# Optimization experiments

Measured on AMD Instinct MI355X. Metric: run time of the kernel, lower is better.

## Reference

```python
import jax, jax.numpy as jnp
import numpy as np


def setup_inputs() -> dict:
    key = jax.random.key(0)
    ks = jax.random.split(key, 7)
    B, P, D = 4, 2048, 1024
    s = 1.0 / np.sqrt(D)
    return {
        "x":  jax.random.normal(ks[0], (B, P, D), dtype=jnp.float32),
        "Wq": jax.random.normal(ks[1], (D, D), dtype=jnp.float32) * s,
        "bq": jnp.zeros((D,), dtype=jnp.float32),
        "Wk": jax.random.normal(ks[2], (D, D), dtype=jnp.float32) * s,
        "bk": jnp.zeros((D,), dtype=jnp.float32),
        "Wv": jax.random.normal(ks[3], (D, D), dtype=jnp.float32) * s,
        "bv": jnp.zeros((D,), dtype=jnp.float32),
    }


def reference(x, Wq, bq, Wk, bk, Wv, bv):
    # x: [B, P, D]; Linear uses W stored torch-style [out, in]: y = x @ W.T + b
    b, p, d = x.shape
    q = jnp.einsum("bpd,ed->bpe", x, Wq) + bq
    k = jnp.einsum("bpd,ed->bpe", x, Wk) + bk
    v = jnp.einsum("bpd,ed->bpe", x, Wv) + bv
    attn = jnp.einsum("bqd,bkd->bqk", q, k)  # [B, P, P]
    causal = jnp.triu(jnp.ones((p, p), dtype=bool), k=1)  # True above diagonal
    attn = jnp.where(causal, -jnp.inf, attn)
    attn = attn / jnp.sqrt(jnp.asarray(d, dtype=attn.dtype))
    scores = jax.nn.softmax(attn, axis=-1)
    # dropout is identity in eval/deterministic mode
    return jnp.einsum("bqk,bkd->bqd", scores, v)
```

## Files before the change

### kernel.cpp

```cpp
#include <hip/hip_runtime.h>
#include <hip/hip_bf16.h>


typedef __attribute__((ext_vector_type(8))) short bf16x8;
typedef __attribute__((ext_vector_type(4))) float f32x4;

__device__ __forceinline__ unsigned short f2bf(float f) {
    union { float f; unsigned u; } v; v.f = f;
    unsigned r = v.u + 0x7FFF + ((v.u >> 16) & 1);
    return (unsigned short)(r >> 16);
}

__device__ __forceinline__ void gload_lds16(const unsigned short* g, unsigned short* l) {
    __builtin_amdgcn_global_load_lds(
        (const __attribute__((address_space(1))) unsigned int*)g,
        (__attribute__((address_space(3))) unsigned int*)l, 16, 0, 0);
}

__global__ void convert_kernel(const float* __restrict__ x,  const float* __restrict__ wq,
                               const float* __restrict__ wk, const float* __restrict__ wv,
                               const float* __restrict__ bq, const float* __restrict__ bk,
                               const float* __restrict__ bv,
                               unsigned short* __restrict__ xb, unsigned short* __restrict__ wqkvb,
                               float* __restrict__ bqkv, float* __restrict__ lsum) {
    long t = (long)blockIdx.x * blockDim.x + threadIdx.x;
    long idx = t * 4;
    const float* src; unsigned short* dst; long off;
    if      (idx <  8388608) { src = x;  dst = xb;            off = idx;            }
    else if (idx <  9437184) { src = wq; dst = wqkvb;         off = idx -  8388608; }
    else if (idx < 10485760) { src = wk; dst = wqkvb+1048576; off = idx -  9437184; }
    else if (idx < 11534336) { src = wv; dst = wqkvb+2097152; off = idx - 10485760; }
    else return;
    float4 v = *(const float4*)(src + off);
    ushort4 o = make_ushort4(f2bf(v.x), f2bf(v.y), f2bf(v.z), f2bf(v.w));
    *(ushort4*)(dst + off) = o;
    if (t < 768) {
        long o2 = t * 4;
        float4 b;
        if      (o2 < 1024) b = *(const float4*)(bq + o2);
        else if (o2 < 2048) b = *(const float4*)(bk + o2 - 1024);
        else                b = *(const float4*)(bv + o2 - 2048);
        *(float4*)(bqkv + o2) = b;
    }
    if (t >= 1024 && t < 3072) {
        float4 z = make_float4(0.f, 0.f, 0.f, 0.f);
        *(float4*)(lsum + (t - 1024) * 4) = z;
    }
}

template<int MODE>
__global__ __launch_bounds__(256)
void gemm_bt(const unsigned short* __restrict__ A, int lda,
             const unsigned short* __restrict__ B, int ldb,
             unsigned short* __restrict__ Cb, float* __restrict__ Cf, int ldc,
             unsigned short* __restrict__ VTb,
             const float* __restrict__ bias_col, float* __restrict__ lsum,
             int K, long bsA, long bsB, long bsC, long bsL) {
    int m0, n0, z;
    if (MODE == 1) {
        const int t = blockIdx.x;
        int i = (int)((sqrtf(8.0f * t + 1.0f) - 1.0f) * 0.5f);
        while ((i + 1) * (i + 2) / 2 <= t) ++i;
        while (i * (i + 1) / 2 > t) --i;
        const int j = t - i * (i + 1) / 2;
        m0 = i * 128; n0 = j * 128; z = blockIdx.y;
    } else {
        n0 = blockIdx.x * 128; m0 = blockIdx.y * 128; z = blockIdx.z;
    }
    A += (long)z * bsA;
    B += (long)z * bsB;
    if (MODE == 2) Cf += (long)z * bsC; else Cb += (long)z * bsC;
    if (MODE != 0) lsum += (long)z * bsL;

    const int Keff = (MODE == 2) ? (m0 + 128) : K;

    __shared__ unsigned short As[128 * 64];
    __shared__ unsigned short Bs[128 * 64];

    const int tid  = threadIdx.x;
    const int lane = tid & 63;
    const int w    = tid >> 6;
    const int wr   = (w >> 1) * 64;
    const int wc   = (w & 1) * 64;
    const int q    = lane >> 4;
    const int ln   = lane & 15;

    const int srow = lane >> 3;
    const int sc   = (lane & 7) ^ srow;
    const unsigned short* gA = A + (long)(m0 + w * 32 + srow) * lda + sc * 8;
    const unsigned short* gB = B + (long)(n0 + w * 32 + srow) * ldb + sc * 8;

    const int pr0 = ((q)     ^ (ln & 7)) * 8;
    const int pr1 = ((q + 4) ^ (ln & 7)) * 8;

    f32x4 acc[4][4] = {};

    for (int k0 = 0; k0 < Keff; k0 += 64) {
        __syncthreads();
#pragma unroll
        for (int s = 0; s < 4; ++s) {
            gload_lds16(gA + k0 + (long)(s * 8) * lda, &As[(w * 32 + s * 8) * 64]);
            gload_lds16(gB + k0 + (long)(s * 8) * ldb, &Bs[(w * 32 + s * 8) * 64]);
        }
        __syncthreads();
#pragma unroll
        for (int kk = 0; kk < 2; ++kk) {
            const int pr = kk ? pr1 : pr0;
            bf16x8 af[4], bfr[4];
#pragma unroll
            for (int i = 0; i < 4; ++i)
                af[i] = *(const bf16x8*)(&As[(wr + i * 16 + ln) * 64 + pr]);
#pragma unroll
            for (int j = 0; j < 4; ++j)
                bfr[j] = *(const bf16x8*)(&Bs[(wc + j * 16 + ln) * 64 + pr]);
#pragma unroll
            for (int i = 0; i < 4; ++i)
#pragma unroll
                for (int j = 0; j < 4; ++j)
                    acc[i][j] = __builtin_amdgcn_mfma_f32_16x16x32_bf16(bfr[j], af[i], acc[i][j], 0, 0, 0);
        }
    }

    if (MODE == 0) {
        if (n0 < 2048) {
#pragma unroll
            for (int j = 0; j < 4; ++j) {
                const float4 bc = *(const float4*)(bias_col + n0 + wc + j * 16 + q * 4);
#pragma unroll
                for (int i = 0; i < 4; ++i) {
                    const int m = m0 + wr + i * 16 + ln;
                    const int n = n0 + wc + j * 16 + q * 4;
                    ushort4 o = make_ushort4(f2bf(acc[i][j][0] + bc.x), f2bf(acc[i][j][1] + bc.y),
                                             f2bf(acc[i][j][2] + bc.z), f2bf(acc[i][j][3] + bc.w));
                    *(ushort4*)(Cb + (long)m * ldc + n) = o;
                }
            }
        } else {
#pragma unroll
            for (int j = 0; j < 4; ++j) {
                const float4 bc = *(const float4*)(bias_col + n0 + wc + j * 16 + q * 4);
                const int e = n0 - 2048 + wc + j * 16 + q * 4;
#pragma unroll
                for (int i = 0; i < 4; ++i) {
                    const int m = m0 + wr + i * 16 + ln;
                    VTb[(long)(e    ) * 8192 + m] = f2bf(acc[i][j][0] + bc.x);
                    VTb[(long)(e + 1) * 8192 + m] = f2bf(acc[i][j][1] + bc.y);
                    VTb[(long)(e + 2) * 8192 + m] = f2bf(acc[i][j][2] + bc.z);
                    VTb[(long)(e + 3) * 8192 + m] = f2bf(acc[i][j][3] + bc.w);
                }
            }
        }
    } else if (MODE == 1) {
        const float scale = 0.03125f;
        float rs[4] = {0.f, 0.f, 0.f, 0.f};
#pragma unroll
        for (int i = 0; i < 4; ++i) {
            const int m = m0 + wr + i * 16 + ln;
#pragma unroll
            for (int j = 0; j < 4; ++j) {
                const int n = n0 + wc + j * 16 + q * 4;
                float p0 = (n     <= m) ? __expf(acc[i][j][0] * scale) : 0.f;
                float p1 = (n + 1 <= m) ? __expf(acc[i][j][1] * scale) : 0.f;
                float p2 = (n + 2 <= m) ? __expf(acc[i][j][2] * scale) : 0.f;
                float p3 = (n + 3 <= m) ? __expf(acc[i][j][3] * scale) : 0.f;
                rs[i] += (p0 + p1) + (p2 + p3);
                ushort4 o = make_ushort4(f2bf(p0), f2bf(p1), f2bf(p2), f2bf(p3));
                *(ushort4*)(Cb + (long)m * ldc + n) = o;
            }
        }
#pragma unroll
        for (int i = 0; i < 4; ++i) {
            float s = rs[i];
            s += __shfl_xor(s, 16); s += __shfl_xor(s, 32);
            if (lane < 16) atomicAdd(&lsum[m0 + wr + i * 16 + ln], s);
        }
    } else {
#pragma unroll
        for (int i = 0; i < 4; ++i) {
            const int m = m0 + wr + i * 16 + ln;
            const float inv = 1.0f / lsum[m];
#pragma unroll
            for (int j = 0; j < 4; ++j) {
                const int n = n0 + wc + j * 16 + q * 4;
                float4 o = make_float4(acc[i][j][0] * inv, acc[i][j][1] * inv,
                                       acc[i][j][2] * inv, acc[i][j][3] * inv);
                *(float4*)(Cf + (long)m * ldc + n) = o;
            }
        }
    }
}

extern "C" void kernel_launch(void* const* d_in, const int* in_sizes, int n_in,
                              void* d_out, int out_size, void* d_ws, size_t ws_size,
                              hipStream_t stream) {
    const float* x  = (const float*)d_in[0];
    const float* Wq = (const float*)d_in[1];
    const float* bq = (const float*)d_in[2];
    const float* Wk = (const float*)d_in[3];
    const float* bk = (const float*)d_in[4];
    const float* Wv = (const float*)d_in[5];
    const float* bv = (const float*)d_in[6];
    float* out = (float*)d_out;

    char* ws = (char*)d_ws;
    unsigned short* xb    = (unsigned short*)ws; ws += (long)8192 * 1024 * 2;
    unsigned short* wqkvb = (unsigned short*)ws; ws += (long)3072 * 1024 * 2;
    float*          bqkv  = (float*)ws;          ws += (long)3072 * 4;
    float*          lsum  = (float*)ws;          ws += (long)8192 * 4;
    unsigned short* QKb   = (unsigned short*)ws; ws += (long)8192 * 2048 * 2;
    unsigned short* VTb   = (unsigned short*)ws; ws += (long)1024 * 8192 * 2;
    unsigned short* Pb    = (unsigned short*)ws; ws += (long)4 * 2048 * 2048 * 2;

    hipLaunchKernelGGL(convert_kernel, dim3(11264), dim3(256), 0, stream,
                       x, Wq, Wk, Wv, bq, bk, bv, xb, wqkvb, bqkv, lsum);

    hipLaunchKernelGGL((gemm_bt<0>), dim3(24, 64, 1), dim3(256), 0, stream,
                       xb, 1024, wqkvb, 1024, QKb, (float*)nullptr, 2048, VTb,
                       bqkv, (float*)nullptr, 1024, 0L, 0L, 0L, 0L);

    hipLaunchKernelGGL((gemm_bt<1>), dim3(136, 4, 1), dim3(256), 0, stream,
                       QKb, 2048, QKb + 1024, 2048, Pb, (float*)nullptr, 2048,
                       (unsigned short*)nullptr, (const float*)nullptr, lsum,
                       1024, (long)2048 * 2048, (long)2048 * 2048, (long)2048 * 2048, 2048L);

    hipLaunchKernelGGL((gemm_bt<2>), dim3(8, 16, 4), dim3(256), 0, stream,
                       Pb, 2048, VTb, 8192, (unsigned short*)nullptr, out, 1024,
                       (unsigned short*)nullptr, (const float*)nullptr, lsum,
                       2048, (long)2048 * 2048, 2048L, (long)2048 * 1024, 2048L);
}
```

Measured before the change: 264.6 us.

## Enlarge GEMM tiles to 256x128 and transpose V via swapped MFMA operands

All three GEMM phases now use 256x128 block tiles, with each wave owning 64 rows across the full 128 columns, so every loaded B fragment is reused across more accumulators. The triangular tile enumeration for the QK^T phase is redone for 256-row strips, and the grids are halved to match. The V projection swaps the MFMA operand order so the transposed result can be written as contiguous ushort4 stores instead of scattered scalar stores. The costs are double the accumulator registers (launch bounds now request 2 blocks), fewer blocks per grid, and coarser causal tiles that compute more masked work on the diagonal.

```diff
diff --git a/kernel.cpp b/kernel.cpp
--- a/kernel.cpp
+++ b/kernel.cpp
@@ -48,8 +48,47 @@
     }
 }
 
+template<bool SWAP>
+__device__ __forceinline__ void kloop(const unsigned short* gA, int lda,
+                                      const unsigned short* gB, int ldb,
+                                      unsigned short* As, unsigned short* Bs,
+                                      int w, int lane, int Keff, f32x4 (&acc)[4][8]) {
+    const int q  = lane >> 4;
+    const int ln = lane & 15;
+    const int pr0 = ((q)     ^ (ln & 7)) * 8;
+    const int pr1 = ((q + 4) ^ (ln & 7)) * 8;
+    for (int k0 = 0; k0 < Keff; k0 += 64) {
+        __syncthreads();
+#pragma unroll
+        for (int s = 0; s < 8; ++s)
+            gload_lds16(gA + k0 + (long)(s * 8) * lda, &As[(w * 64 + s * 8) * 64]);
+#pragma unroll
+        for (int s = 0; s < 4; ++s)
+            gload_lds16(gB + k0 + (long)(s * 8) * ldb, &Bs[(w * 32 + s * 8) * 64]);
+        __syncthreads();
+#pragma unroll
+        for (int kk = 0; kk < 2; ++kk) {
+            const int pr = kk ? pr1 : pr0;
+            bf16x8 af[4], bfr[8];
+#pragma unroll
+            for (int i = 0; i < 4; ++i)
+                af[i] = *(const bf16x8*)(&As[(w * 64 + i * 16 + ln) * 64 + pr]);
+#pragma unroll
+            for (int j = 0; j < 8; ++j)
+                bfr[j] = *(const bf16x8*)(&Bs[(j * 16 + ln) * 64 + pr]);
+#pragma unroll
+            for (int i = 0; i < 4; ++i)
+#pragma unroll
+                for (int j = 0; j < 8; ++j)
+                    acc[i][j] = SWAP
+                        ? __builtin_amdgcn_mfma_f32_16x16x32_bf16(bfr[j], af[i], acc[i][j], 0, 0, 0)
+                        : __builtin_amdgcn_mfma_f32_16x16x32_bf16(af[i], bfr[j], acc[i][j], 0, 0, 0);
+        }
+    }
+}
+
 template<int MODE>
-__global__ __launch_bounds__(256)
+__global__ __launch_bounds__(256, 2)
 void gemm_bt(const unsigned short* __restrict__ A, int lda,
              const unsigned short* __restrict__ B, int ldb,
              unsigned short* __restrict__ Cb, float* __restrict__ Cf, int ldc,
@@ -59,129 +98,97 @@
     int m0, n0, z;
     if (MODE == 1) {
         const int t = blockIdx.x;
-        int i = (int)((sqrtf(8.0f * t + 1.0f) - 1.0f) * 0.5f);
-        while ((i + 1) * (i + 2) / 2 <= t) ++i;
-        while (i * (i + 1) / 2 > t) --i;
-        const int j = t - i * (i + 1) / 2;
-        m0 = i * 128; n0 = j * 128; z = blockIdx.y;
+        int i = (int)sqrtf((float)t);
+        while (i * i + i > t) --i;
+        while ((i + 1) * (i + 1) + (i + 1) <= t) ++i;
+        const int j = t - i * i - i;
+        m0 = i * 256; n0 = j * 128; z = blockIdx.y;
     } else {
-        n0 = blockIdx.x * 128; m0 = blockIdx.y * 128; z = blockIdx.z;
+        n0 = blockIdx.x * 128; m0 = blockIdx.y * 256; z = blockIdx.z;
     }
     A += (long)z * bsA;
     B += (long)z * bsB;
     if (MODE == 2) Cf += (long)z * bsC; else Cb += (long)z * bsC;
     if (MODE != 0) lsum += (long)z * bsL;
 
-    const int Keff = (MODE == 2) ? (m0 + 128) : K;
-
-    __shared__ unsigned short As[128 * 64];
-    __shared__ unsigned short Bs[128 * 64];
+    const int Keff = (MODE == 2) ? (m0 + 256) : K;
+
+    __shared__ __align__(16) unsigned short As[256 * 64];
+    __shared__ __align__(16) unsigned short Bs[128 * 64];
 
     const int tid  = threadIdx.x;
     const int lane = tid & 63;
     const int w    = tid >> 6;
-    const int wr   = (w >> 1) * 64;
-    const int wc   = (w & 1) * 64;
     const int q    = lane >> 4;
     const int ln   = lane & 15;
 
     const int srow = lane >> 3;
     const int sc   = (lane & 7) ^ srow;
-    const unsigned short* gA = A + (long)(m0 + w * 32 + srow) * lda + sc * 8;
+    const unsigned short* gA = A + (long)(m0 + w * 64 + srow) * lda + sc * 8;
     const unsigned short* gB = B + (long)(n0 + w * 32 + srow) * ldb + sc * 8;
 
-    const int pr0 = ((q)     ^ (ln & 7)) * 8;
-    const int pr1 = ((q + 4) ^ (ln & 7)) * 8;
-
-    f32x4 acc[4][4] = {};
-
-    for (int k0 = 0; k0 < Keff; k0 += 64) {
-        __syncthreads();
-#pragma unroll
-        for (int s = 0; s < 4; ++s) {
-            gload_lds16(gA + k0 + (long)(s * 8) * lda, &As[(w * 32 + s * 8) * 64]);
-            gload_lds16(gB + k0 + (long)(s * 8) * ldb, &Bs[(w * 32 + s * 8) * 64]);
-        }
-        __syncthreads();
-#pragma unroll
-        for (int kk = 0; kk < 2; ++kk) {
-            const int pr = kk ? pr1 : pr0;
-            bf16x8 af[4], bfr[4];
-#pragma unroll
-            for (int i = 0; i < 4; ++i)
-                af[i] = *(const bf16x8*)(&As[(wr + i * 16 + ln) * 64 + pr]);
-#pragma unroll
-            for (int j = 0; j < 4; ++j)
-                bfr[j] = *(const bf16x8*)(&Bs[(wc + j * 16 + ln) * 64 + pr]);
-#pragma unroll
-            for (int i = 0; i < 4; ++i)
-#pragma unroll
-                for (int j = 0; j < 4; ++j)
-                    acc[i][j] = __builtin_amdgcn_mfma_f32_16x16x32_bf16(bfr[j], af[i], acc[i][j], 0, 0, 0);
-        }
-    }
+    f32x4 acc[4][8] = {};
+
+    if (MODE == 0 && n0 >= 2048) {
+        kloop<false>(gA, lda, gB, ldb, As, Bs, w, lane, Keff, acc);
+#pragma unroll
+        for (int j = 0; j < 8; ++j) {
+            const int e = n0 - 2048 + j * 16 + ln;
+            const float bc = bias_col[n0 + j * 16 + ln];
+#pragma unroll
+            for (int i = 0; i < 4; ++i) {
+                const int m = m0 + w * 64 + i * 16 + q * 4;
+                ushort4 o = make_ushort4(f2bf(acc[i][j][0] + bc), f2bf(acc[i][j][1] + bc),
+                                         f2bf(acc[i][j][2] + bc), f2bf(acc[i][j][3] + bc));
+                *(ushort4*)(VTb + (long)e * 8192 + m) = o;
+            }
+        }
+        return;
+    }
+
+    kloop<true>(gA, lda, gB, ldb, As, Bs, w, lane, Keff, acc);
 
     if (MODE == 0) {
-        if (n0 < 2048) {
-#pragma unroll
-            for (int j = 0; j < 4; ++j) {
-                const float4 bc = *(const float4*)(bias_col + n0 + wc + j * 16 + q * 4);
-#pragma unroll
-                for (int i = 0; i < 4; ++i) {
-                    const int m = m0 + wr + i * 16 + ln;
-                    const int n = n0 + wc + j * 16 + q * 4;
-                    ushort4 o = make_ushort4(f2bf(acc[i][j][0] + bc.x), f2bf(acc[i][j][1] + bc.y),
-                                             f2bf(acc[i][j][2] + bc.z), f2bf(acc[i][j][3] + bc.w));
-                    *(ushort4*)(Cb + (long)m * ldc + n) = o;
-                }
-            }
-        } else {
-#pragma unroll
-            for (int j = 0; j < 4; ++j) {
-                const float4 bc = *(const float4*)(bias_col + n0 + wc + j * 16 + q * 4);
-                const int e = n0 - 2048 + wc + j * 16 + q * 4;
-#pragma unroll
-                for (int i = 0; i < 4; ++i) {
-                    const int m = m0 + wr + i * 16 + ln;
-                    VTb[(long)(e    ) * 8192 + m] = f2bf(acc[i][j][0] + bc.x);
-                    VTb[(long)(e + 1) * 8192 + m] = f2bf(acc[i][j][1] + bc.y);
-                    VTb[(long)(e + 2) * 8192 + m] = f2bf(acc[i][j][2] + bc.z);
-                    VTb[(long)(e + 3) * 8192 + m] = f2bf(acc[i][j][3] + bc.w);
-                }
+#pragma unroll
+        for (int j = 0; j < 8; ++j) {
+            const float4 bc = *(const float4*)(bias_col + n0 + j * 16 + q * 4);
+#pragma unroll
+            for (int i = 0; i < 4; ++i) {
+                const int m = m0 + w * 64 + i * 16 + ln;
+                const int n = n0 + j * 16 + q * 4;
+                ushort4 o = make_ushort4(f2bf(acc[i][j][0] + bc.x), f2bf(acc[i][j][1] + bc.y),
+                                         f2bf(acc[i][j][2] + bc.z), f2bf(acc[i][j][3] + bc.w));
+                *(ushort4*)(Cb + (long)m * ldc + n) = o;
             }
         }
     } else if (MODE == 1) {
         const float scale = 0.03125f;
-        float rs[4] = {0.f, 0.f, 0.f, 0.f};
 #pragma unroll
         for (int i = 0; i < 4; ++i) {
-            const int m = m0 + wr + i * 16 + ln;
-#pragma unroll
-            for (int j = 0; j < 4; ++j) {
-                const int n = n0 + wc + j * 16 + q * 4;
+            const int m = m0 + w * 64 + i * 16 + ln;
+            float rs = 0.f;
+#pragma unroll
+            for (int j = 0; j < 8; ++j) {
+                const int n = n0 + j * 16 + q * 4;
                 float p0 = (n     <= m) ? __expf(acc[i][j][0] * scale) : 0.f;
                 float p1 = (n + 1 <= m) ? __expf(acc[i][j][1] * scale) : 0.f;
                 float p2 = (n + 2 <= m) ? __expf(acc[i][j][2] * scale) : 0.f;
                 float p3 = (n + 3 <= m) ? __expf(acc[i][j][3] * scale) : 0.f;
-                rs[i] += (p0 + p1) + (p2 + p3);
+                rs += (p0 + p1) + (p2 + p3);
                 ushort4 o = make_ushort4(f2bf(p0), f2bf(p1), f2bf(p2), f2bf(p3));
                 *(ushort4*)(Cb + (long)m * ldc + n) = o;
             }
-        }
+            rs += __shfl_xor(rs, 16); rs += __shfl_xor(rs, 32);
+            if (lane < 16) atomicAdd(&lsum[m], rs);
+        }
+    } else {
 #pragma unroll
         for (int i = 0; i < 4; ++i) {
-            float s = rs[i];
-            s += __shfl_xor(s, 16); s += __shfl_xor(s, 32);
-            if (lane < 16) atomicAdd(&lsum[m0 + wr + i * 16 + ln], s);
-        }
-    } else {
-#pragma unroll
-        for (int i = 0; i < 4; ++i) {
-            const int m = m0 + wr + i * 16 + ln;
+            const int m = m0 + w * 64 + i * 16 + ln;
             const float inv = 1.0f / lsum[m];
 #pragma unroll
-            for (int j = 0; j < 4; ++j) {
-                const int n = n0 + wc + j * 16 + q * 4;
+            for (int j = 0; j < 8; ++j) {
+                const int n = n0 + j * 16 + q * 4;
                 float4 o = make_float4(acc[i][j][0] * inv, acc[i][j][1] * inv,
                                        acc[i][j][2] * inv, acc[i][j][3] * inv);
                 *(float4*)(Cf + (long)m * ldc + n) = o;
@@ -214,16 +221,16 @@
     hipLaunchKernelGGL(convert_kernel, dim3(11264), dim3(256), 0, stream,
                        x, Wq, Wk, Wv, bq, bk, bv, xb, wqkvb, bqkv, lsum);
 
-    hipLaunchKernelGGL((gemm_bt<0>), dim3(24, 64, 1), dim3(256), 0, stream,
+    hipLaunchKernelGGL((gemm_bt<0>), dim3(24, 32, 1), dim3(256), 0, stream,
                        xb, 1024, wqkvb, 1024, QKb, (float*)nullptr, 2048, VTb,
                        bqkv, (float*)nullptr, 1024, 0L, 0L, 0L, 0L);
 
-    hipLaunchKernelGGL((gemm_bt<1>), dim3(136, 4, 1), dim3(256), 0, stream,
+    hipLaunchKernelGGL((gemm_bt<1>), dim3(72, 4, 1), dim3(256), 0, stream,
                        QKb, 2048, QKb + 1024, 2048, Pb, (float*)nullptr, 2048,
                        (unsigned short*)nullptr, (const float*)nullptr, lsum,
                        1024, (long)2048 * 2048, (long)2048 * 2048, (long)2048 * 2048, 2048L);
 
-    hipLaunchKernelGGL((gemm_bt<2>), dim3(8, 16, 4), dim3(256), 0, stream,
+    hipLaunchKernelGGL((gemm_bt<2>), dim3(8, 8, 4), dim3(256), 0, stream,
                        Pb, 2048, VTb, 8192, (unsigned short*)nullptr, out, 1024,
                        (unsigned short*)nullptr, (const float*)nullptr, lsum,
                        2048, (long)2048 * 2048, 2048L, (long)2048 * 1024, 2048L);
```

Result: faster. 254.5 us (-3.8%).

## Double-buffer LDS K-loop, vectorize V-transpose stores, reorder PV tile schedule

Applied to the files above, without the earlier changes.

Splits the templated GEMM into three specialized kernels that share a double-buffered K-loop, so the global-to-LDS load for the next tile overlaps with the MFMAs on the current one and the loop needs fewer barriers. The V projection swaps the MFMA operand order, which lets the transposed V output be written as ushort4 vectors instead of scalar stores. The PV kernel uses a 1D grid that interleaves short and long causal row tiles to balance the triangular workload. The cost is double the LDS per block (64KB), with launch bounds set to 2 blocks per CU.

```diff
diff --git a/kernel.cpp b/kernel.cpp
--- a/kernel.cpp
+++ b/kernel.cpp
@@ -48,144 +48,201 @@
     }
 }
 
-template<int MODE>
-__global__ __launch_bounds__(256)
-void gemm_bt(const unsigned short* __restrict__ A, int lda,
-             const unsigned short* __restrict__ B, int ldb,
-             unsigned short* __restrict__ Cb, float* __restrict__ Cf, int ldc,
-             unsigned short* __restrict__ VTb,
-             const float* __restrict__ bias_col, float* __restrict__ lsum,
-             int K, long bsA, long bsB, long bsC, long bsL) {
-    int m0, n0, z;
-    if (MODE == 1) {
-        const int t = blockIdx.x;
-        int i = (int)((sqrtf(8.0f * t + 1.0f) - 1.0f) * 0.5f);
-        while ((i + 1) * (i + 2) / 2 <= t) ++i;
-        while (i * (i + 1) / 2 > t) --i;
-        const int j = t - i * (i + 1) / 2;
-        m0 = i * 128; n0 = j * 128; z = blockIdx.y;
-    } else {
-        n0 = blockIdx.x * 128; m0 = blockIdx.y * 128; z = blockIdx.z;
-    }
-    A += (long)z * bsA;
-    B += (long)z * bsB;
-    if (MODE == 2) Cf += (long)z * bsC; else Cb += (long)z * bsC;
-    if (MODE != 0) lsum += (long)z * bsL;
-
-    const int Keff = (MODE == 2) ? (m0 + 128) : K;
-
-    __shared__ unsigned short As[128 * 64];
-    __shared__ unsigned short Bs[128 * 64];
-
-    const int tid  = threadIdx.x;
-    const int lane = tid & 63;
-    const int w    = tid >> 6;
-    const int wr   = (w >> 1) * 64;
-    const int wc   = (w & 1) * 64;
-    const int q    = lane >> 4;
-    const int ln   = lane & 15;
-
-    const int srow = lane >> 3;
-    const int sc   = (lane & 7) ^ srow;
-    const unsigned short* gA = A + (long)(m0 + w * 32 + srow) * lda + sc * 8;
-    const unsigned short* gB = B + (long)(n0 + w * 32 + srow) * ldb + sc * 8;
-
+__device__ __forceinline__ void stage(const unsigned short* gA, long lda,
+                                      const unsigned short* gB, long ldb,
+                                      unsigned short* As, unsigned short* Bs,
+                                      int w, int k0) {
+#pragma unroll
+    for (int s = 0; s < 4; ++s) {
+        gload_lds16(gA + k0 + (long)(s * 8) * lda, &As[(w * 32 + s * 8) * 64]);
+        gload_lds16(gB + k0 + (long)(s * 8) * ldb, &Bs[(w * 32 + s * 8) * 64]);
+    }
+}
+
+template<bool SWAP>
+__device__ __forceinline__ void mfma_tile(const unsigned short* As, const unsigned short* Bs,
+                                          int wr, int wc, int ln, int pr0, int pr1,
+                                          f32x4 (&acc)[4][4]) {
+#pragma unroll
+    for (int kk = 0; kk < 2; ++kk) {
+        const int pr = kk ? pr1 : pr0;
+        bf16x8 af[4], bfr[4];
+#pragma unroll
+        for (int i = 0; i < 4; ++i)
+            af[i] = *(const bf16x8*)(&As[(wr + i * 16 + ln) * 64 + pr]);
+#pragma unroll
+        for (int j = 0; j < 4; ++j)
+            bfr[j] = *(const bf16x8*)(&Bs[(wc + j * 16 + ln) * 64 + pr]);
+#pragma unroll
+        for (int i = 0; i < 4; ++i)
+#pragma unroll
+            for (int j = 0; j < 4; ++j)
+                acc[i][j] = SWAP
+                    ? __builtin_amdgcn_mfma_f32_16x16x32_bf16(bfr[j], af[i], acc[i][j], 0, 0, 0)
+                    : __builtin_amdgcn_mfma_f32_16x16x32_bf16(af[i], bfr[j], acc[i][j], 0, 0, 0);
+    }
+}
+
+template<bool SWAP>
+__device__ __forceinline__ void kloop_db(const unsigned short* gA, long lda,
+                                         const unsigned short* gB, long ldb,
+                                         unsigned short* As0, unsigned short* Bs0,
+                                         unsigned short* As1, unsigned short* Bs1,
+                                         int w, int lane, int Keff, f32x4 (&acc)[4][4]) {
+    const int q  = lane >> 4;
+    const int ln = lane & 15;
+    const int wr = (w >> 1) * 64;
+    const int wc = (w & 1) * 64;
     const int pr0 = ((q)     ^ (ln & 7)) * 8;
     const int pr1 = ((q + 4) ^ (ln & 7)) * 8;
-
+    stage(gA, lda, gB, ldb, As0, Bs0, w, 0);
+    __syncthreads();
+    for (int k0 = 0; k0 < Keff; k0 += 128) {
+        stage(gA, lda, gB, ldb, As1, Bs1, w, k0 + 64);
+        mfma_tile<SWAP>(As0, Bs0, wr, wc, ln, pr0, pr1, acc);
+        __syncthreads();
+        if (k0 + 128 < Keff)
+            stage(gA, lda, gB, ldb, As0, Bs0, w, k0 + 128);
+        mfma_tile<SWAP>(As1, Bs1, wr, wc, ln, pr0, pr1, acc);
+        __syncthreads();
+    }
+}
+
+__global__ __launch_bounds__(256, 2)
+void gemm_qkv(const unsigned short* __restrict__ X,
+              const unsigned short* __restrict__ W,
+              unsigned short* __restrict__ QK,
+              unsigned short* __restrict__ VT,
+              const float* __restrict__ bias) {
+    const int n0 = blockIdx.x * 128;
+    const int m0 = blockIdx.y * 128;
+    __shared__ __align__(16) unsigned short As0[128 * 64], Bs0[128 * 64];
+    __shared__ __align__(16) unsigned short As1[128 * 64], Bs1[128 * 64];
+    const int tid = threadIdx.x, lane = tid & 63, w = tid >> 6;
+    const int q = lane >> 4, ln = lane & 15;
+    const int wr = (w >> 1) * 64, wc = (w & 1) * 64;
+    const int srow = lane >> 3, sc = (lane & 7) ^ srow;
+    const unsigned short* gA = X + (long)(m0 + w * 32 + srow) * 1024 + sc * 8;
+    const unsigned short* gB = W + (long)(n0 + w * 32 + srow) * 1024 + sc * 8;
     f32x4 acc[4][4] = {};
-
-    for (int k0 = 0; k0 < Keff; k0 += 64) {
-        __syncthreads();
-#pragma unroll
-        for (int s = 0; s < 4; ++s) {
-            gload_lds16(gA + k0 + (long)(s * 8) * lda, &As[(w * 32 + s * 8) * 64]);
-            gload_lds16(gB + k0 + (long)(s * 8) * ldb, &Bs[(w * 32 + s * 8) * 64]);
-        }
-        __syncthreads();
-#pragma unroll
-        for (int kk = 0; kk < 2; ++kk) {
-            const int pr = kk ? pr1 : pr0;
-            bf16x8 af[4], bfr[4];
-#pragma unroll
-            for (int i = 0; i < 4; ++i)
-                af[i] = *(const bf16x8*)(&As[(wr + i * 16 + ln) * 64 + pr]);
-#pragma unroll
-            for (int j = 0; j < 4; ++j)
-                bfr[j] = *(const bf16x8*)(&Bs[(wc + j * 16 + ln) * 64 + pr]);
-#pragma unroll
-            for (int i = 0; i < 4; ++i)
-#pragma unroll
-                for (int j = 0; j < 4; ++j)
-                    acc[i][j] = __builtin_amdgcn_mfma_f32_16x16x32_bf16(bfr[j], af[i], acc[i][j], 0, 0, 0);
-        }
-    }
-
-    if (MODE == 0) {
-        if (n0 < 2048) {
-#pragma unroll
-            for (int j = 0; j < 4; ++j) {
-                const float4 bc = *(const float4*)(bias_col + n0 + wc + j * 16 + q * 4);
-#pragma unroll
-                for (int i = 0; i < 4; ++i) {
-                    const int m = m0 + wr + i * 16 + ln;
-                    const int n = n0 + wc + j * 16 + q * 4;
-                    ushort4 o = make_ushort4(f2bf(acc[i][j][0] + bc.x), f2bf(acc[i][j][1] + bc.y),
-                                             f2bf(acc[i][j][2] + bc.z), f2bf(acc[i][j][3] + bc.w));
-                    *(ushort4*)(Cb + (long)m * ldc + n) = o;
-                }
+    if (n0 >= 2048) {
+        kloop_db<false>(gA, 1024, gB, 1024, As0, Bs0, As1, Bs1, w, lane, 1024, acc);
+#pragma unroll
+        for (int j = 0; j < 4; ++j) {
+            const int e = n0 - 2048 + wc + j * 16 + ln;
+            const float bc = bias[n0 + wc + j * 16 + ln];
+#pragma unroll
+            for (int i = 0; i < 4; ++i) {
+                const int m = m0 + wr + i * 16 + q * 4;
+                ushort4 o = make_ushort4(f2bf(acc[i][j][0] + bc), f2bf(acc[i][j][1] + bc),
+                                         f2bf(acc[i][j][2] + bc), f2bf(acc[i][j][3] + bc));
+                *(ushort4*)(VT + (long)e * 8192 + m) = o;
             }
-        } else {
-#pragma unroll
-            for (int j = 0; j < 4; ++j) {
-                const float4 bc = *(const float4*)(bias_col + n0 + wc + j * 16 + q * 4);
-                const int e = n0 - 2048 + wc + j * 16 + q * 4;
-#pragma unroll
-                for (int i = 0; i < 4; ++i) {
-                    const int m = m0 + wr + i * 16 + ln;
-                    VTb[(long)(e    ) * 8192 + m] = f2bf(acc[i][j][0] + bc.x);
-                    VTb[(long)(e + 1) * 8192 + m] = f2bf(acc[i][j][1] + bc.y);
-                    VTb[(long)(e + 2) * 8192 + m] = f2bf(acc[i][j][2] + bc.z);
-                    VTb[(long)(e + 3) * 8192 + m] = f2bf(acc[i][j][3] + bc.w);
-                }
+        }
+    } else {
+        kloop_db<true>(gA, 1024, gB, 1024, As0, Bs0, As1, Bs1, w, lane, 1024, acc);
+#pragma unroll
+        for (int j = 0; j < 4; ++j) {
+            const float4 bc = *(const float4*)(bias + n0 + wc + j * 16 + q * 4);
+#pragma unroll
+            for (int i = 0; i < 4; ++i) {
+                const int m = m0 + wr + i * 16 + ln;
+                const int n = n0 + wc + j * 16 + q * 4;
+                ushort4 o = make_ushort4(f2bf(acc[i][j][0] + bc.x), f2bf(acc[i][j][1] + bc.y),
+                                         f2bf(acc[i][j][2] + bc.z), f2bf(acc[i][j][3] + bc.w));
+                *(ushort4*)(QK + (long)m * 2048 + n) = o;
             }
         }
-    } else if (MODE == 1) {
-        const float scale = 0.03125f;
-        float rs[4] = {0.f, 0.f, 0.f, 0.f};
-#pragma unroll
-        for (int i = 0; i < 4; ++i) {
-            const int m = m0 + wr + i * 16 + ln;
-#pragma unroll
-            for (int j = 0; j < 4; ++j) {
-                const int n = n0 + wc + j * 16 + q * 4;
-                float p0 = (n     <= m) ? __expf(acc[i][j][0] * scale) : 0.f;
-                float p1 = (n + 1 <= m) ? __expf(acc[i][j][1] * scale) : 0.f;
-                float p2 = (n + 2 <= m) ? __expf(acc[i][j][2] * scale) : 0.f;
-                float p3 = (n + 3 <= m) ? __expf(acc[i][j][3] * scale) : 0.f;
-                rs[i] += (p0 + p1) + (p2 + p3);
-                ushort4 o = make_ushort4(f2bf(p0), f2bf(p1), f2bf(p2), f2bf(p3));
-                *(ushort4*)(Cb + (long)m * ldc + n) = o;
-            }
-        }
-#pragma unroll
-        for (int i = 0; i < 4; ++i) {
-            float s = rs[i];
-            s += __shfl_xor(s, 16); s += __shfl_xor(s, 32);
-            if (lane < 16) atomicAdd(&lsum[m0 + wr + i * 16 + ln], s);
-        }
-    } else {
-#pragma unroll
-        for (int i = 0; i < 4; ++i) {
-            const int m = m0 + wr + i * 16 + ln;
-            const float inv = 1.0f / lsum[m];
-#pragma unroll
-            for (int j = 0; j < 4; ++j) {
-                const int n = n0 + wc + j * 16 + q * 4;
-                float4 o = make_float4(acc[i][j][0] * inv, acc[i][j][1] * inv,
-                                       acc[i][j][2] * inv, acc[i][j][3] * inv);
-                *(float4*)(Cf + (long)m * ldc + n) = o;
-            }
+    }
+}
+
+__global__ __launch_bounds__(256, 2)
+void gemm_scores(const unsigned short* __restrict__ QK,
+                 unsigned short* __restrict__ P,
+                 float* __restrict__ lsum) {
+    const int t = blockIdx.x;
+    int i = (int)((sqrtf(8.0f * t + 1.0f) - 1.0f) * 0.5f);
+    while ((i + 1) * (i + 2) / 2 <= t) ++i;
+    while (i * (i + 1) / 2 > t) --i;
+    const int j = t - i * (i + 1) / 2;
+    const int m0 = i * 128, n0 = j * 128, z = blockIdx.y;
+    const unsigned short* Qz = QK + (long)z * 2048 * 2048;
+    const unsigned short* Kz = Qz + 1024;
+    unsigned short* Pz = P + (long)z * 2048 * 2048;
+    float* lz = lsum + z * 2048;
+
+    __shared__ __align__(16) unsigned short As0[128 * 64], Bs0[128 * 64];
+    __shared__ __align__(16) unsigned short As1[128 * 64], Bs1[128 * 64];
+    const int tid = threadIdx.x, lane = tid & 63, w = tid >> 6;
+    const int q = lane >> 4, ln = lane & 15;
+    const int wr = (w >> 1) * 64, wc = (w & 1) * 64;
+    const int srow = lane >> 3, sc = (lane & 7) ^ srow;
+    const unsigned short* gA = Qz + (long)(m0 + w * 32 + srow) * 2048 + sc * 8;
+    const unsigned short* gB = Kz + (long)(n0 + w * 32 + srow) * 2048 + sc * 8;
+    f32x4 acc[4][4] = {};
+    kloop_db<true>(gA, 2048, gB, 2048, As0, Bs0, As1, Bs1, w, lane, 1024, acc);
+
+    const float scale = 0.03125f;
+#pragma unroll
+    for (int i2 = 0; i2 < 4; ++i2) {
+        const int m = m0 + wr + i2 * 16 + ln;
+        float rs = 0.f;
+#pragma unroll
+        for (int j2 = 0; j2 < 4; ++j2) {
+            const int n = n0 + wc + j2 * 16 + q * 4;
+            float p0 = (n     <= m) ? __expf(acc[i2][j2][0] * scale) : 0.f;
+            float p1 = (n + 1 <= m) ? __expf(acc[i2][j2][1] * scale) : 0.f;
+            float p2 = (n + 2 <= m) ? __expf(acc[i2][j2][2] * scale) : 0.f;
+            float p3 = (n + 3 <= m) ? __expf(acc[i2][j2][3] * scale) : 0.f;
+            rs += (p0 + p1) + (p2 + p3);
+            ushort4 o = make_ushort4(f2bf(p0), f2bf(p1), f2bf(p2), f2bf(p3));
+            *(ushort4*)(Pz + (long)m * 2048 + n) = o;
+        }
+        rs += __shfl_xor(rs, 16); rs += __shfl_xor(rs, 32);
+        if (lane < 16) atomicAdd(&lz[m], rs);
+    }
+}
+
+__global__ __launch_bounds__(256, 2)
+void gemm_pv(const unsigned short* __restrict__ P,
+             const unsigned short* __restrict__ VT,
+             const float* __restrict__ lsum,
+             float* __restrict__ out) {
+    const int L  = blockIdx.x;
+    const int ph = L >> 8;
+    const int c  = L & 255;
+    const int z  = c >> 6;
+    const int r  = c & 63;
+    const int mh = r >> 3;
+    const int nt = r & 7;
+    const int mt = ph ? 15 - mh : mh;
+    const int m0 = mt * 128, n0 = nt * 128;
+    const int Keff = m0 + 128;
+    const unsigned short* Pz = P + (long)z * 2048 * 2048;
+    const unsigned short* Vz = VT + (long)z * 2048;
+    const float* lz = lsum + z * 2048;
+
+    __shared__ __align__(16) unsigned short As0[128 * 64], Bs0[128 * 64];
+    __shared__ __align__(16) unsigned short As1[128 * 64], Bs1[128 * 64];
+    const int tid = threadIdx.x, lane = tid & 63, w = tid >> 6;
+    const int q = lane >> 4, ln = lane & 15;
+    const int wr = (w >> 1) * 64, wc = (w & 1) * 64;
+    const int srow = lane >> 3, sc = (lane & 7) ^ srow;
+    const unsigned short* gA = Pz + (long)(m0 + w * 32 + srow) * 2048 + sc * 8;
+    const unsigned short* gB = Vz + (long)(n0 + w * 32 + srow) * 8192 + sc * 8;
+    f32x4 acc[4][4] = {};
+    kloop_db<true>(gA, 2048, gB, 8192, As0, Bs0, As1, Bs1, w, lane, Keff, acc);
+
+#pragma unroll
+    for (int i2 = 0; i2 < 4; ++i2) {
+        const int m = m0 + wr + i2 * 16 + ln;
+        const float inv = 1.0f / lz[m];
+#pragma unroll
+        for (int j2 = 0; j2 < 4; ++j2) {
+            const int n = n0 + wc + j2 * 16 + q * 4;
+            float4 o = make_float4(acc[i2][j2][0] * inv, acc[i2][j2][1] * inv,
+                                   acc[i2][j2][2] * inv, acc[i2][j2][3] * inv);
+            *(float4*)(out + (long)(z * 2048 + m) * 1024 + n) = o;
         }
     }
 }
@@ -214,17 +271,12 @@
     hipLaunchKernelGGL(convert_kernel, dim3(11264), dim3(256), 0, stream,
                        x, Wq, Wk, Wv, bq, bk, bv, xb, wqkvb, bqkv, lsum);
 
-    hipLaunchKernelGGL((gemm_bt<0>), dim3(24, 64, 1), dim3(256), 0, stream,
-                       xb, 1024, wqkvb, 1024, QKb, (float*)nullptr, 2048, VTb,
-                       bqkv, (float*)nullptr, 1024, 0L, 0L, 0L, 0L);
-
-    hipLaunchKernelGGL((gemm_bt<1>), dim3(136, 4, 1), dim3(256), 0, stream,
-                       QKb, 2048, QKb + 1024, 2048, Pb, (float*)nullptr, 2048,
-                       (unsigned short*)nullptr, (const float*)nullptr, lsum,
-                       1024, (long)2048 * 2048, (long)2048 * 2048, (long)2048 * 2048, 2048L);
-
-    hipLaunchKernelGGL((gemm_bt<2>), dim3(8, 16, 4), dim3(256), 0, stream,
-                       Pb, 2048, VTb, 8192, (unsigned short*)nullptr, out, 1024,
-                       (unsigned short*)nullptr, (const float*)nullptr, lsum,
-                       2048, (long)2048 * 2048, 2048L, (long)2048 * 1024, 2048L);
-}
+    hipLaunchKernelGGL(gemm_qkv, dim3(24, 64, 1), dim3(256), 0, stream,
+                       xb, wqkvb, QKb, VTb, bqkv);
+
+    hipLaunchKernelGGL(gemm_scores, dim3(136, 4, 1), dim3(256), 0, stream,
+                       QKb, Pb, lsum);
+
+    hipLaunchKernelGGL(gemm_pv, dim3(512, 1, 1), dim3(256), 0, stream,
+                       Pb, VTb, lsum, out);
+}
```

Measured after the change: 242.6 us. 8.3% less time.
